# Performance work log

Measured on AMD Instinct MI355X. Metric: run time of the kernel, lower is better.

Reference implementation:

```python
import jax, jax.numpy as jnp
import numpy as np

B, S, D = 4, 2048, 512   # batch, seq_len, hidden_size
H, HD = 1, 512           # num_heads (must be 1 given the view), head_size
ALPHA, BW, A = 2.0, 512.0, 0.5
EPS = 1e-12              # F.normalize / cdist-grad stabilizer


def setup_inputs() -> dict:
    key = jax.random.key(0)
    ks = jax.random.split(key, 7)
    s = 1.0 / np.sqrt(D)  # keep q,k,v at unit scale like trained weights
    return {
        "x": jax.random.normal(ks[0], (B, S, D), jnp.float32),
        "Wq": jax.random.normal(ks[1], (HD, D), jnp.float32) * s,
        "bq": jax.random.normal(ks[2], (HD,), jnp.float32) * 0.01,
        "Wk": jax.random.normal(ks[3], (HD, D), jnp.float32) * s,
        "bk": jax.random.normal(ks[4], (HD,), jnp.float32) * 0.01,
        "Wv": jax.random.normal(ks[5], (HD, D), jnp.float32) * s,
        "bv": jax.random.normal(ks[6], (HD,), jnp.float32) * 0.01,
    }


def reference(x, Wq, bq, Wk, bk, Wv, bv):
    # projections, then (B, H, S, HD)
    q = (x @ Wq.T + bq).reshape(B, S, H, HD).transpose(0, 2, 1, 3)
    k = (x @ Wk.T + bk).reshape(B, S, H, HD).transpose(0, 2, 1, 3)
    v = (x @ Wv.T + bv).reshape(B, S, H, HD).transpose(0, 2, 1, 3)

    # torch.cdist(q, k, p=2): pairwise Euclidean distance, shape (B, H, S, S)
    sq = ((q * q).sum(-1)[..., :, None]
          + (k * k).sum(-1)[..., None, :]
          - 2.0 * jnp.einsum('bhsd,bhtd->bhst', q, k))
    g_dist = jnp.sqrt(jnp.maximum(sq, EPS))

    # alpha >= 2 branch: exp(-(g / sqrt(bw))**(alpha/(alpha-1)))
    attn_score = jnp.exp(-(g_dist / jnp.sqrt(BW)) ** (ALPHA / (ALPHA - 1.0)))

    # bistochastic (Sinkhorn-like) renormalization, a > 0 branch
    N_R = attn_score.sum(-1)   # row sums  (B, H, S)
    N_C = attn_score.sum(-2)   # col sums  (B, H, S)
    K_tilde = (N_R ** (-A))[..., :, None] * attn_score * (N_C ** (-A))[..., None, :]

    # F.normalize(K_tilde, p=1, dim=3); entries are nonnegative so |.| == .
    probs = K_tilde / jnp.maximum(K_tilde.sum(-1, keepdims=True), EPS)

    # dropout prob = 0.0 -> identity
    out = jnp.einsum('bhst,bhtd->bhsd', probs, v)
    return out, probs
```

## Files before the change

### kernel.cpp

```cpp
#include <hip/hip_runtime.h>
#include <hip/hip_bf16.h>

typedef short short8 __attribute__((ext_vector_type(8)));
typedef short short4v __attribute__((ext_vector_type(4)));
typedef float f32x4 __attribute__((ext_vector_type(4)));

#define S_LEN 2048
#define DIM   512
#define NBATCH 4

typedef unsigned short ushort_t;

__device__ __forceinline__ float b2f(unsigned short u) {
    union { unsigned u; float f; } x; x.u = ((unsigned)u) << 16; return x.f;
}
__device__ __forceinline__ unsigned short f2b(float f) {
    union { float f; unsigned u; } x; x.f = f;
    unsigned r = x.u + 0x7FFFu + ((x.u >> 16) & 1u);
    return (unsigned short)(r >> 16);
}
__device__ __forceinline__ float wave_sum(float v) {
    #pragma unroll
    for (int off = 32; off > 0; off >>= 1) v += __shfl_xor(v, off, 64);
    return v;
}
__device__ __forceinline__ void gld16(const void* g, void* l) {
    __builtin_amdgcn_global_load_lds(
        (const __attribute__((address_space(1))) unsigned int*)g,
        (__attribute__((address_space(3))) unsigned int*)l, 16, 0, 0);
}

__global__ void convert_kernel(const float* __restrict__ x,
                               const float* __restrict__ Wq,
                               const float* __restrict__ Wk,
                               const float* __restrict__ Wv,
                               ushort_t* __restrict__ xb,
                               ushort_t* __restrict__ Wb)
{
    const int blk = blockIdx.x;
    const float* src;
    ushort_t* dst;
    size_t off;
    if (blk < 2048) {
        src = x; dst = xb; off = (size_t)blk * 2048;
    } else {
        int w = (blk - 2048) >> 7;
        int r = (blk - 2048) & 127;
        src = (w == 0) ? Wq : (w == 1) ? Wk : Wv;
        dst = Wb + (size_t)w * DIM * DIM;
        off = (size_t)r * 2048;
    }
    size_t i = off + (size_t)threadIdx.x * 8;
    f32x4 a = *(const f32x4*)&src[i];
    f32x4 c = *(const f32x4*)&src[i + 4];
    short8 o;
    #pragma unroll
    for (int e = 0; e < 4; e++) {
        o[e]     = (short)f2b(a[e]);
        o[4 + e] = (short)f2b(c[e]);
    }
    *(short8*)&dst[i] = o;
}

__global__ void proj_kernel(
    const ushort_t* __restrict__ xb,
    const ushort_t* __restrict__ Wb,
    const float* __restrict__ bq, const float* __restrict__ bk,
    const float* __restrict__ bv,
    ushort_t* __restrict__ Q, ushort_t* __restrict__ Kp,
    ushort_t* __restrict__ Vt)
{
    __shared__ __align__(16) ushort_t As[128 * 32];
    __shared__ __align__(16) ushort_t Bs[128 * 32];
    const int z = blockIdx.z;
    const ushort_t* A  = xb;
    const ushort_t* Bt = Wb + (size_t)z * DIM * DIM;
    const float* bias = (z == 0) ? bq : (z == 1) ? bk : bv;

    const int bm0 = blockIdx.x * 128, bn0 = blockIdx.y * 128;
    const int tid = threadIdx.x;
    const int lane = tid & 63, wave = tid >> 6;
    const int wm = wave >> 1, wn = wave & 1;
    const int quad = lane >> 4;
    const int mrow = wm * 64 + (lane & 15);
    const int ncol = wn * 64 + (lane & 15);
    f32x4 acc[4][4] = {};

    for (int k0 = 0; k0 < DIM; k0 += 32) {
        __syncthreads();
        #pragma unroll
        for (int u = 0; u < 2; u++) {
            int f = u * 256 + tid;
            int row = f >> 2, c4 = (f & 3) ^ ((row >> 1) & 3);
            gld16(&A[(size_t)(bm0 + row) * DIM + k0 + c4 * 8],
                  &As[(u * 256 + wave * 64) * 8]);
        }
        #pragma unroll
        for (int u = 0; u < 2; u++) {
            int f = u * 256 + tid;
            int row = f >> 2, c4 = (f & 3) ^ ((row >> 1) & 3);
            gld16(&Bt[(size_t)(bn0 + row) * DIM + k0 + c4 * 8],
                  &Bs[(u * 256 + wave * 64) * 8]);
        }
        __syncthreads();

        short8 af[4], bf[4];
        #pragma unroll
        for (int i = 0; i < 4; i++) {
            int row = mrow + 16 * i;
            af[i] = *(const short8*)&As[row * 32 + (quad ^ ((row >> 1) & 3)) * 8];
        }
        #pragma unroll
        for (int j = 0; j < 4; j++) {
            int row = ncol + 16 * j;
            bf[j] = *(const short8*)&Bs[row * 32 + (quad ^ ((row >> 1) & 3)) * 8];
        }
        #pragma unroll
        for (int i = 0; i < 4; i++)
            #pragma unroll
            for (int j = 0; j < 4; j++)
                acc[i][j] = __builtin_amdgcn_mfma_f32_16x16x32_bf16(
                    af[i], bf[j], acc[i][j], 0, 0, 0);
    }

    if (z < 2) {
        ushort_t* O = (z == 0) ? Q : Kp;
        #pragma unroll
        for (int j = 0; j < 4; j++) {
            int gcol = bn0 + wn * 64 + 16 * j + (lane & 15);
            float bb = bias[gcol];
            #pragma unroll
            for (int i = 0; i < 4; i++)
                #pragma unroll
                for (int r = 0; r < 4; r++) {
                    int grow = bm0 + wm * 64 + 16 * i + quad * 4 + r;
                    O[(size_t)grow * DIM + gcol] = f2b(acc[i][j][r] + bb);
                }
        }
    } else {
        #pragma unroll
        for (int j = 0; j < 4; j++) {
            int gcol = bn0 + wn * 64 + 16 * j + (lane & 15);
            float bb = bias[gcol];
            #pragma unroll
            for (int i = 0; i < 4; i++) {
                int grow0 = bm0 + wm * 64 + 16 * i + quad * 4;
                int bb2 = grow0 >> 11, s = grow0 & 2047;
                short4v o4;
                #pragma unroll
                for (int r = 0; r < 4; r++) o4[r] = (short)f2b(acc[i][j][r] + bb);
                *(short4v*)&Vt[((size_t)bb2 * DIM + gcol) * S_LEN + s] = o4;
            }
        }
    }
}

__global__ void norms_kernel(const ushort_t* __restrict__ Q,
                             const ushort_t* __restrict__ Kp,
                             float* __restrict__ nq, float* __restrict__ nk)
{
    const int wave = threadIdx.x >> 6, lane = threadIdx.x & 63;
    const int row = blockIdx.x * 4 + wave;
    const ushort_t* src = (blockIdx.y == 0) ? Q : Kp;
    float* dst = (blockIdx.y == 0) ? nq : nk;
    short8 v = *(const short8*)&src[(size_t)row * DIM + lane * 8];
    float s = 0.f;
    #pragma unroll
    for (int e = 0; e < 8; e++) { float f = b2f((ushort_t)v[e]); s += f * f; }
    s = wave_sum(s);
    if (lane == 0) dst[row] = s;
}

__global__ void score_kernel(const ushort_t* __restrict__ Q,
                             const ushort_t* __restrict__ Kp,
                             const float* __restrict__ nq,
                             const float* __restrict__ nk,
                             ushort_t* __restrict__ attnb,
                             float* __restrict__ NC)
{
    __shared__ __align__(16) ushort_t As[128 * 32];
    __shared__ __align__(16) ushort_t Bs[128 * 32];
    const int b = blockIdx.z;
    const ushort_t* A  = Q  + (size_t)b * S_LEN * DIM;
    const ushort_t* Bt = Kp + (size_t)b * S_LEN * DIM;
    const int bm0 = blockIdx.x * 128, bn0 = blockIdx.y * 128;
    const int tid = threadIdx.x;
    const int lane = tid & 63, wave = tid >> 6;
    const int wm = wave >> 1, wn = wave & 1;
    const int quad = lane >> 4;
    const int mrow = wm * 64 + (lane & 15);
    const int ncol = wn * 64 + (lane & 15);
    f32x4 acc[4][4] = {};

    for (int k0 = 0; k0 < DIM; k0 += 32) {
        __syncthreads();
        #pragma unroll
        for (int u = 0; u < 2; u++) {
            int f = u * 256 + tid;
            int row = f >> 2, c4 = (f & 3) ^ ((row >> 1) & 3);
            gld16(&A[(size_t)(bm0 + row) * DIM + k0 + c4 * 8],
                  &As[(u * 256 + wave * 64) * 8]);
        }
        #pragma unroll
        for (int u = 0; u < 2; u++) {
            int f = u * 256 + tid;
            int row = f >> 2, c4 = (f & 3) ^ ((row >> 1) & 3);
            gld16(&Bt[(size_t)(bn0 + row) * DIM + k0 + c4 * 8],
                  &Bs[(u * 256 + wave * 64) * 8]);
        }
        __syncthreads();

        short8 af[4], bf[4];
        #pragma unroll
        for (int i = 0; i < 4; i++) {
            int row = mrow + 16 * i;
            af[i] = *(const short8*)&As[row * 32 + (quad ^ ((row >> 1) & 3)) * 8];
        }
        #pragma unroll
        for (int j = 0; j < 4; j++) {
            int row = ncol + 16 * j;
            bf[j] = *(const short8*)&Bs[row * 32 + (quad ^ ((row >> 1) & 3)) * 8];
        }
        #pragma unroll
        for (int i = 0; i < 4; i++)
            #pragma unroll
            for (int j = 0; j < 4; j++)
                acc[i][j] = __builtin_amdgcn_mfma_f32_16x16x32_bf16(
                    af[i], bf[j], acc[i][j], 0, 0, 0);
    }

    ushort_t* ob = attnb + (size_t)b * S_LEN * S_LEN;
    float nqv[16], nkv[4];
    #pragma unroll
    for (int i = 0; i < 4; i++)
        #pragma unroll
        for (int r = 0; r < 4; r++)
            nqv[i * 4 + r] = nq[b * S_LEN + bm0 + wm * 64 + 16 * i + quad * 4 + r];
    #pragma unroll
    for (int j = 0; j < 4; j++)
        nkv[j] = nk[b * S_LEN + bn0 + wn * 64 + 16 * j + (lane & 15)];

    float cp[4] = {0.f, 0.f, 0.f, 0.f};
    #pragma unroll
    for (int i = 0; i < 4; i++)
        #pragma unroll
        for (int j = 0; j < 4; j++)
            #pragma unroll
            for (int r = 0; r < 4; r++) {
                int grow = bm0 + wm * 64 + 16 * i + quad * 4 + r;
                int gcol = bn0 + wn * 64 + 16 * j + (lane & 15);
                float sq = nqv[i * 4 + r] + nkv[j] - 2.0f * acc[i][j][r];
                sq = fmaxf(sq, 1e-12f);
                ushort_t ub = f2b(__expf(sq * (-1.0f / 512.0f)));
                ob[(size_t)grow * S_LEN + gcol] = ub;
                cp[j] += b2f(ub);
            }
    #pragma unroll
    for (int j = 0; j < 4; j++) {
        float v = cp[j];
        v += __shfl_xor(v, 16, 64);
        v += __shfl_xor(v, 32, 64);
        if (quad == 0) {
            int gcol = bn0 + wn * 64 + 16 * j + (lane & 15);
            atomicAdd(&NC[b * S_LEN + gcol], v);
        }
    }
}

__global__ void scale_vt_kernel(ushort_t* __restrict__ Vt,
                                const float* __restrict__ NC)
{
    size_t idx = ((size_t)blockIdx.x * 256 + threadIdx.x) * 8;
    int s0 = (int)(idx & 2047);
    int b  = (int)(idx >> 20);
    const float* cb = NC + (b << 11);
    short8 v = *(short8*)&Vt[idx];
    #pragma unroll
    for (int e = 0; e < 8; e++)
        v[e] = (short)f2b(b2f((ushort_t)v[e]) * rsqrtf(cb[s0 + e]));
    *(short8*)&Vt[idx] = v;
}

__global__ void rowsumprobs_kernel(const ushort_t* __restrict__ attnb,
                                   const float* __restrict__ NC,
                                   float* __restrict__ probs,
                                   float* __restrict__ rr)
{
    __shared__ float red[4];
    const int s = blockIdx.x, b = blockIdx.y;
    const size_t R = (size_t)b * S_LEN + s;
    const ushort_t* row = attnb + R * S_LEN;
    const float* cb = NC + (b << 11);
    const int t = threadIdx.x * 8;
    const int wave = threadIdx.x >> 6, lane = threadIdx.x & 63;

    short8 av = *(const short8*)&row[t];
    float pv[8], acc = 0.f;
    #pragma unroll
    for (int e = 0; e < 8; e++) {
        pv[e] = b2f((ushort_t)av[e]) * rsqrtf(cb[t + e]);
        acc += pv[e];
    }
    acc = wave_sum(acc);
    if (lane == 0) red[wave] = acc;
    __syncthreads();
    float rs = 1.0f / (red[0] + red[1] + red[2] + red[3]);

    float* prow = probs + R * S_LEN;
    f32x4 o0, o1;
    #pragma unroll
    for (int e = 0; e < 4; e++) { o0[e] = pv[e] * rs; o1[e] = pv[4 + e] * rs; }
    *(f32x4*)&prow[t] = o0;
    *(f32x4*)&prow[t + 4] = o1;
    if (threadIdx.x == 0) rr[R] = rs;
}

__global__ void out_gemm_kernel(const ushort_t* __restrict__ attnb,
                                const ushort_t* __restrict__ Vtc,
                                const float* __restrict__ rr,
                                float* __restrict__ outp)
{
    __shared__ __align__(16) ushort_t As[128 * 32];
    __shared__ __align__(16) ushort_t Bs[128 * 32];
    const int b = blockIdx.z;
    const ushort_t* A  = attnb + (size_t)b * S_LEN * S_LEN;
    const ushort_t* Bt = Vtc + (size_t)b * DIM * S_LEN;
    const int bm0 = blockIdx.x * 128, bn0 = blockIdx.y * 128;
    const int tid = threadIdx.x;
    const int lane = tid & 63, wave = tid >> 6;
    const int wm = wave >> 1, wn = wave & 1;
    const int quad = lane >> 4;
    const int mrow = wm * 64 + (lane & 15);
    const int ncol = wn * 64 + (lane & 15);
    f32x4 acc[4][4] = {};

    for (int k0 = 0; k0 < S_LEN; k0 += 32) {
        __syncthreads();
        #pragma unroll
        for (int u = 0; u < 2; u++) {
            int f = u * 256 + tid;
            int row = f >> 2, c4 = (f & 3) ^ ((row >> 1) & 3);
            gld16(&A[(size_t)(bm0 + row) * S_LEN + k0 + c4 * 8],
                  &As[(u * 256 + wave * 64) * 8]);
        }
        #pragma unroll
        for (int u = 0; u < 2; u++) {
            int f = u * 256 + tid;
            int row = f >> 2, c4 = (f & 3) ^ ((row >> 1) & 3);
            gld16(&Bt[(size_t)(bn0 + row) * S_LEN + k0 + c4 * 8],
                  &Bs[(u * 256 + wave * 64) * 8]);
        }
        __syncthreads();

        short8 af[4], bf[4];
        #pragma unroll
        for (int i = 0; i < 4; i++) {
            int row = mrow + 16 * i;
            af[i] = *(const short8*)&As[row * 32 + (quad ^ ((row >> 1) & 3)) * 8];
        }
        #pragma unroll
        for (int j = 0; j < 4; j++) {
            int row = ncol + 16 * j;
            bf[j] = *(const short8*)&Bs[row * 32 + (quad ^ ((row >> 1) & 3)) * 8];
        }
        #pragma unroll
        for (int i = 0; i < 4; i++)
            #pragma unroll
            for (int j = 0; j < 4; j++)
                acc[i][j] = __builtin_amdgcn_mfma_f32_16x16x32_bf16(
                    af[i], bf[j], acc[i][j], 0, 0, 0);
    }

    float* C = outp + (size_t)b * S_LEN * DIM;
    float rv[16];
    #pragma unroll
    for (int i = 0; i < 4; i++)
        #pragma unroll
        for (int r = 0; r < 4; r++)
            rv[i * 4 + r] = rr[b * S_LEN + bm0 + wm * 64 + 16 * i + quad * 4 + r];
    #pragma unroll
    for (int j = 0; j < 4; j++) {
        int gcol = bn0 + wn * 64 + 16 * j + (lane & 15);
        #pragma unroll
        for (int i = 0; i < 4; i++)
            #pragma unroll
            for (int r = 0; r < 4; r++) {
                int grow = bm0 + wm * 64 + 16 * i + quad * 4 + r;
                C[(size_t)grow * DIM + gcol] = acc[i][j][r] * rv[i * 4 + r];
            }
    }
}

extern "C" void kernel_launch(void* const* d_in, const int* in_sizes, int n_in,
                              void* d_out, int out_size, void* d_ws, size_t ws_size,
                              hipStream_t stream)
{
    const float* x  = (const float*)d_in[0];
    const float* Wq = (const float*)d_in[1];
    const float* bq = (const float*)d_in[2];
    const float* Wk = (const float*)d_in[3];
    const float* bk = (const float*)d_in[4];
    const float* Wv = (const float*)d_in[5];
    const float* bv = (const float*)d_in[6];

    float* out   = (float*)d_out;
    float* probs = out + (size_t)NBATCH * S_LEN * DIM;

    ushort_t* Qb = (ushort_t*)d_out;
    ushort_t* Kb = Qb + (size_t)8192 * DIM;
    ushort_t* xb = (ushort_t*)probs;
    ushort_t* Wb = xb + (size_t)8192 * DIM;
    ushort_t* Vt    = (ushort_t*)d_ws;
    ushort_t* attnb = Vt + (size_t)NBATCH * DIM * S_LEN;
    float* nq = (float*)(attnb + (size_t)NBATCH * S_LEN * S_LEN);
    float* nk = nq + 8192;
    float* NC = nk + 8192;
    float* cc = NC + 8192;
    float* rr = cc + 8192;

    hipMemsetAsync(NC, 0, 8192 * sizeof(float), stream);

    convert_kernel<<<2432, 256, 0, stream>>>(x, Wq, Wk, Wv, xb, Wb);
    proj_kernel<<<dim3(64, 4, 3), 256, 0, stream>>>(xb, Wb, bq, bk, bv,
                                                    Qb, Kb, Vt);
    norms_kernel<<<dim3(2048, 2), 256, 0, stream>>>(Qb, Kb, nq, nk);
    score_kernel<<<dim3(16, 16, NBATCH), 256, 0, stream>>>(Qb, Kb, nq, nk,
                                                           attnb, NC);
    scale_vt_kernel<<<2048, 256, 0, stream>>>(Vt, NC);
    rowsumprobs_kernel<<<dim3(S_LEN, NBATCH), 256, 0, stream>>>(attnb, NC,
                                                                probs, rr);
    out_gemm_kernel<<<dim3(16, 4, NBATCH), 256, 0, stream>>>(attnb, Vt, rr, out);
}
```

Before: 211.3 us.

## Triple-buffer LDS in GEMM kernels and make row-normalise one wave per row

```diff
diff --git a/kernel.cpp b/kernel.cpp
--- a/kernel.cpp
+++ b/kernel.cpp
@@ -10,6 +10,10 @@
 #define NBATCH 4
 
 typedef unsigned short ushort_t;
+
+#define WAITV(n) asm volatile("s_waitcnt vmcnt(" #n ")" ::: "memory")
+#define BARRIER() do { __builtin_amdgcn_s_barrier(); \
+                       asm volatile("" ::: "memory"); } while (0)
 
 __device__ __forceinline__ float b2f(unsigned short u) {
     union { unsigned u; float f; } x; x.u = ((unsigned)u) << 16; return x.f;
@@ -70,8 +74,8 @@
     ushort_t* __restrict__ Q, ushort_t* __restrict__ Kp,
     ushort_t* __restrict__ Vt)
 {
-    __shared__ __align__(16) ushort_t As[128 * 32];
-    __shared__ __align__(16) ushort_t Bs[128 * 32];
+    __shared__ __align__(16) ushort_t As[3][128 * 32];
+    __shared__ __align__(16) ushort_t Bs[3][128 * 32];
     const int z = blockIdx.z;
     const ushort_t* A  = xb;
     const ushort_t* Bt = Wb + (size_t)z * DIM * DIM;
@@ -86,34 +90,40 @@
     const int ncol = wn * 64 + (lane & 15);
     f32x4 acc[4][4] = {};
 
-    for (int k0 = 0; k0 < DIM; k0 += 32) {
-        __syncthreads();
+    auto stage = [&](int sb, int k0) {
         #pragma unroll
         for (int u = 0; u < 2; u++) {
             int f = u * 256 + tid;
             int row = f >> 2, c4 = (f & 3) ^ ((row >> 1) & 3);
             gld16(&A[(size_t)(bm0 + row) * DIM + k0 + c4 * 8],
-                  &As[(u * 256 + wave * 64) * 8]);
+                  &As[sb][(u * 256 + wave * 64) * 8]);
         }
         #pragma unroll
         for (int u = 0; u < 2; u++) {
             int f = u * 256 + tid;
             int row = f >> 2, c4 = (f & 3) ^ ((row >> 1) & 3);
             gld16(&Bt[(size_t)(bn0 + row) * DIM + k0 + c4 * 8],
-                  &Bs[(u * 256 + wave * 64) * 8]);
-        }
-        __syncthreads();
-
+                  &Bs[sb][(u * 256 + wave * 64) * 8]);
+        }
+    };
+
+    stage(0, 0);
+    stage(1, 32);
+    int cur = 0;
+    for (int t = 0; t < 16; t++) {
+        if (t < 15) { WAITV(4); } else { WAITV(0); }
+        BARRIER();
+        if (t + 2 < 16) stage((t + 2) % 3, (t + 2) * 32);
         short8 af[4], bf[4];
         #pragma unroll
         for (int i = 0; i < 4; i++) {
             int row = mrow + 16 * i;
-            af[i] = *(const short8*)&As[row * 32 + (quad ^ ((row >> 1) & 3)) * 8];
+            af[i] = *(const short8*)&As[cur][row * 32 + (quad ^ ((row >> 1) & 3)) * 8];
         }
         #pragma unroll
         for (int j = 0; j < 4; j++) {
             int row = ncol + 16 * j;
-            bf[j] = *(const short8*)&Bs[row * 32 + (quad ^ ((row >> 1) & 3)) * 8];
+            bf[j] = *(const short8*)&Bs[cur][row * 32 + (quad ^ ((row >> 1) & 3)) * 8];
         }
         #pragma unroll
         for (int i = 0; i < 4; i++)
@@ -121,6 +131,7 @@
             for (int j = 0; j < 4; j++)
                 acc[i][j] = __builtin_amdgcn_mfma_f32_16x16x32_bf16(
                     af[i], bf[j], acc[i][j], 0, 0, 0);
+        cur = (cur + 1 == 3) ? 0 : cur + 1;
     }
 
     if (z < 2) {
@@ -178,8 +189,8 @@
                              ushort_t* __restrict__ attnb,
                              float* __restrict__ NC)
 {
-    __shared__ __align__(16) ushort_t As[128 * 32];
-    __shared__ __align__(16) ushort_t Bs[128 * 32];
+    __shared__ __align__(16) ushort_t As[3][128 * 32];
+    __shared__ __align__(16) ushort_t Bs[3][128 * 32];
     const int b = blockIdx.z;
     const ushort_t* A  = Q  + (size_t)b * S_LEN * DIM;
     const ushort_t* Bt = Kp + (size_t)b * S_LEN * DIM;
@@ -192,34 +203,40 @@
     const int ncol = wn * 64 + (lane & 15);
     f32x4 acc[4][4] = {};
 
-    for (int k0 = 0; k0 < DIM; k0 += 32) {
-        __syncthreads();
+    auto stage = [&](int sb, int k0) {
         #pragma unroll
         for (int u = 0; u < 2; u++) {
             int f = u * 256 + tid;
             int row = f >> 2, c4 = (f & 3) ^ ((row >> 1) & 3);
             gld16(&A[(size_t)(bm0 + row) * DIM + k0 + c4 * 8],
-                  &As[(u * 256 + wave * 64) * 8]);
+                  &As[sb][(u * 256 + wave * 64) * 8]);
         }
         #pragma unroll
         for (int u = 0; u < 2; u++) {
             int f = u * 256 + tid;
             int row = f >> 2, c4 = (f & 3) ^ ((row >> 1) & 3);
             gld16(&Bt[(size_t)(bn0 + row) * DIM + k0 + c4 * 8],
-                  &Bs[(u * 256 + wave * 64) * 8]);
-        }
-        __syncthreads();
-
+                  &Bs[sb][(u * 256 + wave * 64) * 8]);
+        }
+    };
+
+    stage(0, 0);
+    stage(1, 32);
+    int cur = 0;
+    for (int t = 0; t < 16; t++) {
+        if (t < 15) { WAITV(4); } else { WAITV(0); }
+        BARRIER();
+        if (t + 2 < 16) stage((t + 2) % 3, (t + 2) * 32);
         short8 af[4], bf[4];
         #pragma unroll
         for (int i = 0; i < 4; i++) {
             int row = mrow + 16 * i;
-            af[i] = *(const short8*)&As[row * 32 + (quad ^ ((row >> 1) & 3)) * 8];
+            af[i] = *(const short8*)&As[cur][row * 32 + (quad ^ ((row >> 1) & 3)) * 8];
         }
         #pragma unroll
         for (int j = 0; j < 4; j++) {
             int row = ncol + 16 * j;
-            bf[j] = *(const short8*)&Bs[row * 32 + (quad ^ ((row >> 1) & 3)) * 8];
+            bf[j] = *(const short8*)&Bs[cur][row * 32 + (quad ^ ((row >> 1) & 3)) * 8];
         }
         #pragma unroll
         for (int i = 0; i < 4; i++)
@@ -227,6 +244,7 @@
             for (int j = 0; j < 4; j++)
                 acc[i][j] = __builtin_amdgcn_mfma_f32_16x16x32_bf16(
                     af[i], bf[j], acc[i][j], 0, 0, 0);
+        cur = (cur + 1 == 3) ? 0 : cur + 1;
     }
 
     ushort_t* ob = attnb + (size_t)b * S_LEN * S_LEN;
@@ -286,33 +304,36 @@
                                    float* __restrict__ probs,
                                    float* __restrict__ rr)
 {
-    __shared__ float red[4];
-    const int s = blockIdx.x, b = blockIdx.y;
+    const int wave = threadIdx.x >> 6, lane = threadIdx.x & 63;
+    const int s = blockIdx.x * 8 + wave, b = blockIdx.y;
     const size_t R = (size_t)b * S_LEN + s;
     const ushort_t* row = attnb + R * S_LEN;
     const float* cb = NC + (b << 11);
-    const int t = threadIdx.x * 8;
-    const int wave = threadIdx.x >> 6, lane = threadIdx.x & 63;
-
-    short8 av = *(const short8*)&row[t];
-    float pv[8], acc = 0.f;
-    #pragma unroll
-    for (int e = 0; e < 8; e++) {
-        pv[e] = b2f((ushort_t)av[e]) * rsqrtf(cb[t + e]);
-        acc += pv[e];
-    }
-    acc = wave_sum(acc);
-    if (lane == 0) red[wave] = acc;
-    __syncthreads();
-    float rs = 1.0f / (red[0] + red[1] + red[2] + red[3]);
+
+    float pv[4][8], acc = 0.f;
+    #pragma unroll
+    for (int c = 0; c < 4; c++) {
+        int t = c * 512 + lane * 8;
+        short8 av = *(const short8*)&row[t];
+        #pragma unroll
+        for (int e = 0; e < 8; e++) {
+            pv[c][e] = b2f((ushort_t)av[e]) * rsqrtf(cb[t + e]);
+            acc += pv[c][e];
+        }
+    }
+    float rs = 1.0f / wave_sum(acc);
 
     float* prow = probs + R * S_LEN;
-    f32x4 o0, o1;
-    #pragma unroll
-    for (int e = 0; e < 4; e++) { o0[e] = pv[e] * rs; o1[e] = pv[4 + e] * rs; }
-    *(f32x4*)&prow[t] = o0;
-    *(f32x4*)&prow[t + 4] = o1;
-    if (threadIdx.x == 0) rr[R] = rs;
+    #pragma unroll
+    for (int c = 0; c < 4; c++) {
+        int t = c * 512 + lane * 8;
+        f32x4 o0, o1;
+        #pragma unroll
+        for (int e = 0; e < 4; e++) { o0[e] = pv[c][e] * rs; o1[e] = pv[c][4 + e] * rs; }
+        __builtin_nontemporal_store(o0, (f32x4*)&prow[t]);
+        __builtin_nontemporal_store(o1, (f32x4*)&prow[t + 4]);
+    }
+    if (lane == 0) rr[R] = rs;
 }
 
 __global__ void out_gemm_kernel(const ushort_t* __restrict__ attnb,
@@ -320,8 +341,8 @@
                                 const float* __restrict__ rr,
                                 float* __restrict__ outp)
 {
-    __shared__ __align__(16) ushort_t As[128 * 32];
-    __shared__ __align__(16) ushort_t Bs[128 * 32];
+    __shared__ __align__(16) ushort_t As[3][128 * 32];
+    __shared__ __align__(16) ushort_t Bs[3][128 * 32];
     const int b = blockIdx.z;
     const ushort_t* A  = attnb + (size_t)b * S_LEN * S_LEN;
     const ushort_t* Bt = Vtc + (size_t)b * DIM * S_LEN;
@@ -334,34 +355,40 @@
     const int ncol = wn * 64 + (lane & 15);
     f32x4 acc[4][4] = {};
 
-    for (int k0 = 0; k0 < S_LEN; k0 += 32) {
-        __syncthreads();
+    auto stage = [&](int sb, int k0) {
         #pragma unroll
         for (int u = 0; u < 2; u++) {
             int f = u * 256 + tid;
             int row = f >> 2, c4 = (f & 3) ^ ((row >> 1) & 3);
             gld16(&A[(size_t)(bm0 + row) * S_LEN + k0 + c4 * 8],
-                  &As[(u * 256 + wave * 64) * 8]);
+                  &As[sb][(u * 256 + wave * 64) * 8]);
         }
         #pragma unroll
         for (int u = 0; u < 2; u++) {
             int f = u * 256 + tid;
             int row = f >> 2, c4 = (f & 3) ^ ((row >> 1) & 3);
             gld16(&Bt[(size_t)(bn0 + row) * S_LEN + k0 + c4 * 8],
-                  &Bs[(u * 256 + wave * 64) * 8]);
-        }
-        __syncthreads();
-
+                  &Bs[sb][(u * 256 + wave * 64) * 8]);
+        }
+    };
+
+    stage(0, 0);
+    stage(1, 32);
+    int cur = 0;
+    for (int t = 0; t < 64; t++) {
+        if (t < 63) { WAITV(4); } else { WAITV(0); }
+        BARRIER();
+        if (t + 2 < 64) stage((t + 2) % 3, (t + 2) * 32);
         short8 af[4], bf[4];
         #pragma unroll
         for (int i = 0; i < 4; i++) {
             int row = mrow + 16 * i;
-            af[i] = *(const short8*)&As[row * 32 + (quad ^ ((row >> 1) & 3)) * 8];
+            af[i] = *(const short8*)&As[cur][row * 32 + (quad ^ ((row >> 1) & 3)) * 8];
         }
         #pragma unroll
         for (int j = 0; j < 4; j++) {
             int row = ncol + 16 * j;
-            bf[j] = *(const short8*)&Bs[row * 32 + (quad ^ ((row >> 1) & 3)) * 8];
+            bf[j] = *(const short8*)&Bs[cur][row * 32 + (quad ^ ((row >> 1) & 3)) * 8];
         }
         #pragma unroll
         for (int i = 0; i < 4; i++)
@@ -369,6 +396,7 @@
             for (int j = 0; j < 4; j++)
                 acc[i][j] = __builtin_amdgcn_mfma_f32_16x16x32_bf16(
                     af[i], bf[j], acc[i][j], 0, 0, 0);
+        cur = (cur + 1 == 3) ? 0 : cur + 1;
     }
 
     float* C = outp + (size_t)b * S_LEN * DIM;
@@ -386,7 +414,8 @@
             #pragma unroll
             for (int r = 0; r < 4; r++) {
                 int grow = bm0 + wm * 64 + 16 * i + quad * 4 + r;
-                C[(size_t)grow * DIM + gcol] = acc[i][j][r] * rv[i * 4 + r];
+                __builtin_nontemporal_store(acc[i][j][r] * rv[i * 4 + r],
+                                            &C[(size_t)grow * DIM + gcol]);
             }
     }
 }
@@ -427,7 +456,7 @@
     score_kernel<<<dim3(16, 16, NBATCH), 256, 0, stream>>>(Qb, Kb, nq, nk,
                                                            attnb, NC);
     scale_vt_kernel<<<2048, 256, 0, stream>>>(Vt, NC);
-    rowsumprobs_kernel<<<dim3(S_LEN, NBATCH), 256, 0, stream>>>(attnb, NC,
-                                                                probs, rr);
+    rowsumprobs_kernel<<<dim3(256, NBATCH), 512, 0, stream>>>(attnb, NC,
+                                                              probs, rr);
     out_gemm_kernel<<<dim3(16, 4, NBATCH), 256, 0, stream>>>(attnb, Vt, rr, out);
 }
```

Result: slower. 223.1 us (+5.6%).
